# Performance work log

Hardware: AMD Instinct MI355X
Metric: run time of the kernel (lower is better)

The kernel has to match this reference:

```python
import jax, jax.numpy as jnp
import numpy as np
from jax import lax

B, T, C = 64, 50000, 4
MSYN, D, PATCH = 4, 160, 25
K_ENV, K_BUR, K_PRE = 25, 9, 9
DN = ('NCW', 'OIW', 'NCW')


def _dwconv(x, w, pad):
    # depthwise conv1d, x: [B,C,T], w: [C,1,K]
    return lax.conv_general_dilated(x, w, (1,), [(pad, pad)],
                                    dimension_numbers=DN,
                                    feature_group_count=x.shape[1])


def setup_inputs() -> dict:
    key = jax.random.key(0)
    ks = jax.random.split(key, 8)
    X = jax.random.normal(ks[0], (B, T, C), dtype=jnp.float32)
    M = jnp.ones((B, T, C), dtype=jnp.float32)
    s = 0.1
    w_env = jax.random.normal(ks[1], (C, 1, K_ENV), dtype=jnp.float32) * s
    w_burst = jax.random.normal(ks[2], (C, 1, K_BUR), dtype=jnp.float32) * s
    synergy_raw = jax.random.normal(ks[3], (MSYN, C), dtype=jnp.float32) * s
    w_pre_dw = jax.random.normal(ks[4], (MSYN, 1, K_PRE), dtype=jnp.float32) * s
    w_pre_pw = jax.random.normal(ks[5], (MSYN, MSYN, 1), dtype=jnp.float32) * s
    w_proj = jax.random.normal(ks[6], (D, MSYN, PATCH), dtype=jnp.float32) * s
    ln_gamma = jnp.ones((D,), dtype=jnp.float32)
    ln_beta = jnp.zeros((D,), dtype=jnp.float32)
    return {"X": X, "M": M, "w_env": w_env, "w_burst": w_burst,
            "synergy_raw": synergy_raw, "w_pre_dw": w_pre_dw,
            "w_pre_pw": w_pre_pw, "w_proj": w_proj,
            "ln_gamma": ln_gamma, "ln_beta": ln_beta}


def reference(X, M, w_env, w_burst, synergy_raw, w_pre_dw, w_pre_pw, w_proj, ln_gamma, ln_beta):
    # x: [B,C,T]
    x = (X * M).transpose(0, 2, 1)
    env = _dwconv(jnp.abs(x), w_env, K_ENV // 2)
    dx = jnp.pad(x[:, :, 1:] - x[:, :, :-1], ((0, 0), (0, 0), (1, 0)))
    burst = _dwconv(jnp.abs(dx), w_burst, K_BUR // 2)
    xm = 0.9 * env + 0.6 * burst + 0.2 * x
    # row-normalized softplus synergy matrix [Msyn, C]
    W = jax.nn.softplus(synergy_raw)
    W = W / jnp.maximum(W.sum(axis=1, keepdims=True), 1e-6)
    S = jnp.einsum('mc,bct->bmt', W, xm)
    Mm = (M.transpose(0, 2, 1) > 0).astype(x.dtype)
    Sm = jnp.clip(jnp.einsum('mc,bct->bmt', W, Mm), 0.0, 1.0)
    # pre: depthwise conv k=9 -> GELU -> 1x1 conv -> GELU (dropout = identity in eval)
    S = jax.nn.gelu(_dwconv(S, w_pre_dw, K_PRE // 2), approximate=False)
    S = jax.nn.gelu(jnp.einsum('om,bmt->bot', w_pre_pw[:, :, 0], S), approximate=False)
    S = S.transpose(0, 2, 1)          # [B,T,Msyn]
    Sm = Sm.transpose(0, 2, 1)        # [B,T,Msyn]
    # PatchProject1D
    p = PATCH
    T2 = (S.shape[1] // p) * p
    S = S[:, :T2, :]
    Sm = Sm[:, :T2, :]
    xs = (S * Sm).transpose(0, 2, 1)  # [B,Msyn,T2]
    h = lax.conv_general_dilated(xs, w_proj, (p,), 'VALID',
                                 dimension_numbers=DN).transpose(0, 2, 1)  # [B,L,D]
    mu = h.mean(axis=-1, keepdims=True)
    var = ((h - mu) ** 2).mean(axis=-1, keepdims=True)
    h = (h - mu) * lax.rsqrt(var + 1e-5) * ln_gamma + ln_beta
    # patchify time mask
    m_time = (Sm.mean(axis=-1) > 0).astype(jnp.float32)       # [B,T2]
    L = T2 // p
    m_patch = (m_time.reshape(Sm.shape[0], L, p).mean(axis=-1) > 0.1).astype(jnp.float32)
    return (h, m_patch)
```

## Files before the change

kernel.cpp:

```cpp
#include <hip/hip_runtime.h>
#include <hip/hip_bf16.h>
#include <cstddef>

#define T_LEN 50000

typedef __attribute__((ext_vector_type(8))) short bf16x8;
typedef __attribute__((ext_vector_type(4))) float f32x4;

__device__ __forceinline__ float sp_(float x){ return (x > 20.f) ? x : log1pf(expf(x)); }
__device__ __forceinline__ float gelu1(float x){ return 0.5f*x*(1.f + erff(x*0.7071067811865475f)); }

__global__ void k_cvtw(const float* __restrict__ wproj, __hip_bfloat16* __restrict__ wbf)
{
    int idx = blockIdx.x*256 + threadIdx.x;
    if (idx < 160*128) {
        int d = idx >> 7, i = idx & 127;
        float v = (i < 100) ? wproj[d*100 + i] : 0.f;
        wbf[idx] = __float2bfloat16(v);
    }
}

__global__ __launch_bounds__(256) void k_pre(
    const float* __restrict__ X, const float* __restrict__ Mq,
    const float* __restrict__ w_env, const float* __restrict__ w_bur,
    const float* __restrict__ syn, const float* __restrict__ wdw,
    const float* __restrict__ wpw,
    __hip_bfloat16* __restrict__ xs_out, float* __restrict__ mpatch)
{
    __shared__ float4 xb[1290];
    __shared__ float4 s1b[1134];
    __shared__ unsigned char maskb[1032];
    __shared__ float WnL[16];
    __shared__ float4 SmLUT[16];
    __shared__ __align__(16) __hip_bfloat16 abf[40*128];

    const int tid  = threadIdx.x;
    const int b    = blockIdx.x / 50;
    const int tile = blockIdx.x % 50;
    const int t0   = tile * 1000;

    const float4* X4 = (const float4*)X + (size_t)b * T_LEN;
    const float4* M4 = (const float4*)Mq + (size_t)b * T_LEN;
    #pragma unroll
    for (int jj = 0; jj < 5; ++jj) {
        int idx = tid + jj*256;
        if (idx < 1032) {
            int t = t0 - 16 + idx;
            float4 xv = make_float4(0.f,0.f,0.f,0.f);
            unsigned mk = 0u;
            if (t >= 0 && t < T_LEN) {
                float4 a = X4[t], m = M4[t];
                xv = make_float4(a.x*m.x, a.y*m.y, a.z*m.z, a.w*m.w);
                mk = (m.x>0.f?1u:0u) | (m.y>0.f?2u:0u) | (m.z>0.f?4u:0u) | (m.w>0.f?8u:0u);
            }
            xb[idx + (idx>>2)] = xv;
            maskb[idx] = (unsigned char)mk;
        }
    }
    for (int idx = tid; idx < 40*28; idx += 256) {
        int p = idx / 28, i = 100 + idx % 28;
        abf[p*128 + i] = __float2bfloat16(0.f);
    }
    if (tid < 4) {
        float w0 = sp_(syn[tid*4+0]), w1 = sp_(syn[tid*4+1]);
        float w2 = sp_(syn[tid*4+2]), w3 = sp_(syn[tid*4+3]);
        float inv = 1.f / fmaxf(w0+w1+w2+w3, 1e-6f);
        WnL[tid*4+0]=w0*inv; WnL[tid*4+1]=w1*inv; WnL[tid*4+2]=w2*inv; WnL[tid*4+3]=w3*inv;
    }
    __syncthreads();
    if (tid < 16) {
        float sm[4];
        #pragma unroll
        for (int m=0;m<4;++m) {
            float a = 0.f;
            #pragma unroll
            for (int c=0;c<4;++c) if (tid & (1<<c)) a += WnL[m*4+c];
            sm[m] = fminf(a, 1.f);
        }
        SmLUT[tid] = make_float4(sm[0],sm[1],sm[2],sm[3]);
    }

    if (tid < 252) {
        float4 env[4], bur[4], xk[4];
        #pragma unroll
        for (int j=0;j<4;++j){ env[j]=make_float4(0,0,0,0); bur[j]=make_float4(0,0,0,0); }
        float4 xprev = make_float4(0,0,0,0);
        const int base  = 4*tid;
        const int gbase = t0 - 4 + 4*tid;
        #pragma unroll
        for (int s = -12; s <= 15; ++s) {
            int lt = base + (s+12);
            float4 xc = xb[lt + (lt>>2)];
            float4 ax = make_float4(fabsf(xc.x),fabsf(xc.y),fabsf(xc.z),fabsf(xc.w));
            if (s >= -4 && s <= 7) {
                int g = gbase + s;
                float4 dx;
                if (g <= 0 || g >= T_LEN) dx = make_float4(0,0,0,0);
                else dx = make_float4(xc.x-xprev.x, xc.y-xprev.y, xc.z-xprev.z, xc.w-xprev.w);
                float4 adx = make_float4(fabsf(dx.x),fabsf(dx.y),fabsf(dx.z),fabsf(dx.w));
                #pragma unroll
                for (int j=0;j<4;++j) {
                    int bk = s + 4 - j;
                    if (bk >= 0 && bk < 9) {
                        float b0=w_bur[bk], b1=w_bur[9+bk], b2=w_bur[18+bk], b3=w_bur[27+bk];
                        bur[j].x = fmaf(b0, adx.x, bur[j].x);
                        bur[j].y = fmaf(b1, adx.y, bur[j].y);
                        bur[j].z = fmaf(b2, adx.z, bur[j].z);
                        bur[j].w = fmaf(b3, adx.w, bur[j].w);
                    }
                }
            }
            #pragma unroll
            for (int j=0;j<4;++j) {
                int k = s + 12 - j;
                if (k >= 0 && k < 25) {
                    float e0=w_env[k], e1=w_env[25+k], e2=w_env[50+k], e3=w_env[75+k];
                    env[j].x = fmaf(e0, ax.x, env[j].x);
                    env[j].y = fmaf(e1, ax.y, env[j].y);
                    env[j].z = fmaf(e2, ax.z, env[j].z);
                    env[j].w = fmaf(e3, ax.w, env[j].w);
                }
            }
            if (s >= 0 && s <= 3) xk[s] = xc;
            xprev = xc;
        }
        #pragma unroll
        for (int j=0;j<4;++j) {
            int g = gbase + j;
            float4 xm = make_float4(
                0.9f*env[j].x + 0.6f*bur[j].x + 0.2f*xk[j].x,
                0.9f*env[j].y + 0.6f*bur[j].y + 0.2f*xk[j].y,
                0.9f*env[j].z + 0.6f*bur[j].z + 0.2f*xk[j].z,
                0.9f*env[j].w + 0.6f*bur[j].w + 0.2f*xk[j].w);
            float4 out = make_float4(0,0,0,0);
            if (g >= 0 && g < T_LEN) {
                out.x = WnL[0]*xm.x  + WnL[1]*xm.y  + WnL[2]*xm.z  + WnL[3]*xm.w;
                out.y = WnL[4]*xm.x  + WnL[5]*xm.y  + WnL[6]*xm.z  + WnL[7]*xm.w;
                out.z = WnL[8]*xm.x  + WnL[9]*xm.y  + WnL[10]*xm.z + WnL[11]*xm.w;
                out.w = WnL[12]*xm.x + WnL[13]*xm.y + WnL[14]*xm.z + WnL[15]*xm.w;
            }
            int ls = base + j;
            s1b[ls + (ls>>3)] = out;
        }
    }
    __syncthreads();

    if (tid < 250) {
        float4 s2a[4];
        #pragma unroll
        for (int j=0;j<4;++j) s2a[j]=make_float4(0,0,0,0);
        const int base = 4*tid;
        #pragma unroll
        for (int s = -4; s <= 7; ++s) {
            int ls = base + s + 4;
            float4 sc = s1b[ls + (ls>>3)];
            #pragma unroll
            for (int j=0;j<4;++j) {
                int k = s + 4 - j;
                if (k >= 0 && k < 9) {
                    float d0=wdw[k], d1=wdw[9+k], d2=wdw[18+k], d3=wdw[27+k];
                    s2a[j].x = fmaf(d0, sc.x, s2a[j].x);
                    s2a[j].y = fmaf(d1, sc.y, s2a[j].y);
                    s2a[j].z = fmaf(d2, sc.z, s2a[j].z);
                    s2a[j].w = fmaf(d3, sc.w, s2a[j].w);
                }
            }
        }
        #pragma unroll
        for (int j=0;j<4;++j) {
            int t = base + j;
            float g0 = gelu1(s2a[j].x), g1 = gelu1(s2a[j].y);
            float g2 = gelu1(s2a[j].z), g3 = gelu1(s2a[j].w);
            float4 sm = SmLUT[maskb[t + 16]];
            int p = t / 25, k = t % 25;
            float smv[4] = {sm.x, sm.y, sm.z, sm.w};
            #pragma unroll
            for (int o=0;o<4;++o) {
                float v = wpw[o*4+0]*g0 + wpw[o*4+1]*g1 + wpw[o*4+2]*g2 + wpw[o*4+3]*g3;
                abf[p*128 + o*25 + k] = __float2bfloat16(gelu1(v) * smv[o]);
            }
        }
    }
    __syncthreads();

    {
        const float4* src = (const float4*)abf;
        float4* dst = (float4*)(xs_out + (size_t)(b*2000 + tile*40)*128);
        #pragma unroll
        for (int it = 0; it < 3; ++it) {
            int idx = tid + it*256;
            if (idx < 640) dst[idx] = src[idx];
        }
    }
    if (tid < 40) {
        int cnt = 0;
        #pragma unroll
        for (int k=0;k<25;++k) cnt += (maskb[16 + tid*25 + k] != 0) ? 1 : 0;
        mpatch[(size_t)b*2000 + tile*40 + tid] = (cnt >= 3) ? 1.f : 0.f;
    }
}

__global__ __launch_bounds__(256) void k_proj(
    const __hip_bfloat16* __restrict__ wbf, const __hip_bfloat16* __restrict__ xsg,
    const float* __restrict__ gamma, const float* __restrict__ beta,
    float* __restrict__ hout)
{
    __shared__ __align__(16) unsigned short Wl[160*136];
    __shared__ __align__(16) unsigned short Al[64*136];
    const int tid  = threadIdx.x;
    const int wv   = tid >> 6, lane = tid & 63;
    const int n    = lane & 15, quad = lane >> 4;

    {
        const float4* wg = (const float4*)wbf;
        #pragma unroll
        for (int it = 0; it < 10; ++it) {
            int idx = tid + it*256;
            int row = idx >> 4, cir = idx & 15;
            *(float4*)(Wl + row*136 + cir*8) = wg[idx];
        }
    }

    for (int bt = 0; bt < 2; ++bt) {
        const int p0 = (blockIdx.x*2 + bt) * 64;
        __syncthreads();
        {
            const float4* ag = (const float4*)(xsg + (size_t)p0*128);
            #pragma unroll
            for (int it = 0; it < 4; ++it) {
                int idx = tid + it*256;
                int row = idx >> 4, cir = idx & 15;
                *(float4*)(Al + row*136 + cir*8) = ag[idx];
            }
        }
        __syncthreads();

        f32x4 acc[10];
        #pragma unroll
        for (int t = 0; t < 10; ++t) acc[t] = (f32x4){0.f,0.f,0.f,0.f};
        #pragma unroll
        for (int kk = 0; kk < 4; ++kk) {
            bf16x8 pf = *(const bf16x8*)(Al + (wv*16 + n)*136 + kk*32 + quad*8);
            #pragma unroll
            for (int t = 0; t < 10; ++t) {
                bf16x8 wf = *(const bf16x8*)(Wl + (t*16 + n)*136 + kk*32 + quad*8);
                acc[t] = __builtin_amdgcn_mfma_f32_16x16x32_bf16(wf, pf, acc[t], 0, 0, 0);
            }
        }

        float s = 0.f;
        #pragma unroll
        for (int t = 0; t < 10; ++t) {
            #pragma unroll
            for (int r = 0; r < 4; ++r) s += acc[t][r];
        }
        s += __shfl_xor(s, 16, 64); s += __shfl_xor(s, 32, 64);
        const float mu = s * (1.f/160.f);
        float q = 0.f;
        #pragma unroll
        for (int t = 0; t < 10; ++t) {
            #pragma unroll
            for (int r = 0; r < 4; ++r) { float dv = acc[t][r] - mu; q = fmaf(dv, dv, q); }
        }
        q += __shfl_xor(q, 16, 64); q += __shfl_xor(q, 32, 64);
        const float rs = rsqrtf(q * (1.f/160.f) + 1e-5f);

        const int prow = p0 + wv*16 + n;
        float* hp = hout + (size_t)prow*160;
        #pragma unroll
        for (int t = 0; t < 10; ++t) {
            const float4 g  = *(const float4*)(gamma + t*16 + quad*4);
            const float4 be = *(const float4*)(beta  + t*16 + quad*4);
            float4 o;
            o.x = (acc[t][0] - mu)*rs*g.x + be.x;
            o.y = (acc[t][1] - mu)*rs*g.y + be.y;
            o.z = (acc[t][2] - mu)*rs*g.z + be.z;
            o.w = (acc[t][3] - mu)*rs*g.w + be.w;
            *(float4*)(hp + t*16 + quad*4) = o;
        }
    }
}

extern "C" void kernel_launch(void* const* d_in, const int* in_sizes, int n_in,
                              void* d_out, int out_size, void* d_ws, size_t ws_size,
                              hipStream_t stream) {
    const float* X     = (const float*)d_in[0];
    const float* M     = (const float*)d_in[1];
    const float* w_env = (const float*)d_in[2];
    const float* w_bur = (const float*)d_in[3];
    const float* syn   = (const float*)d_in[4];
    const float* wdw   = (const float*)d_in[5];
    const float* wpw   = (const float*)d_in[6];
    const float* wproj = (const float*)d_in[7];
    const float* gam   = (const float*)d_in[8];
    const float* bet   = (const float*)d_in[9];

    float* h      = (float*)d_out;
    float* mpatch = h + (size_t)64*2000*160;

    __hip_bfloat16* wbf = (__hip_bfloat16*)d_ws;
    __hip_bfloat16* xsb = (__hip_bfloat16*)((char*)d_ws + 65536);

    k_cvtw<<<80, 256, 0, stream>>>(wproj, wbf);
    k_pre<<<3200, 256, 0, stream>>>(X, M, w_env, w_bur, syn, wdw, wpw, xsb, mpatch);
    k_proj<<<1000, 256, 0, stream>>>(wbf, xsb, gam, bet, h);
}
```

Before: 257.5 us.

## Fuse patch projection and LayerNorm into the preprocessing kernel

```diff
diff --git a/kernel.cpp b/kernel.cpp
--- a/kernel.cpp
+++ b/kernel.cpp
@@ -20,19 +20,22 @@
     }
 }
 
-__global__ __launch_bounds__(256) void k_pre(
+__global__ __launch_bounds__(256, 2) void k_fused(
     const float* __restrict__ X, const float* __restrict__ Mq,
     const float* __restrict__ w_env, const float* __restrict__ w_bur,
     const float* __restrict__ syn, const float* __restrict__ wdw,
-    const float* __restrict__ wpw,
-    __hip_bfloat16* __restrict__ xs_out, float* __restrict__ mpatch)
+    const float* __restrict__ wpw, const __hip_bfloat16* __restrict__ wbf,
+    const float* __restrict__ gamma, const float* __restrict__ beta,
+    float* __restrict__ hout, float* __restrict__ mpatch)
 {
     __shared__ float4 xb[1290];
     __shared__ float4 s1b[1134];
     __shared__ unsigned char maskb[1032];
     __shared__ float WnL[16];
     __shared__ float4 SmLUT[16];
-    __shared__ __align__(16) __hip_bfloat16 abf[40*128];
+    __shared__ __align__(16) __hip_bfloat16 abf[48*136];
+    __shared__ float partS[4][3][16];
+    __shared__ float partQ[4][3][16];
 
     const int tid  = threadIdx.x;
     const int b    = blockIdx.x / 50;
@@ -57,9 +60,11 @@
             maskb[idx] = (unsigned char)mk;
         }
     }
-    for (int idx = tid; idx < 40*28; idx += 256) {
-        int p = idx / 28, i = 100 + idx % 28;
-        abf[p*128 + i] = __float2bfloat16(0.f);
+    for (int idx = tid; idx < 1120 + 1024; idx += 256) {
+        int p, i;
+        if (idx < 1120) { p = idx / 28; i = 100 + idx % 28; }
+        else { int j = idx - 1120; p = 40 + (j >> 7); i = j & 127; }
+        abf[p*136 + i] = __float2bfloat16(0.f);
     }
     if (tid < 4) {
         float w0 = sp_(syn[tid*4+0]), w1 = sp_(syn[tid*4+1]);
@@ -177,107 +182,116 @@
             #pragma unroll
             for (int o=0;o<4;++o) {
                 float v = wpw[o*4+0]*g0 + wpw[o*4+1]*g1 + wpw[o*4+2]*g2 + wpw[o*4+3]*g3;
-                abf[p*128 + o*25 + k] = __float2bfloat16(gelu1(v) * smv[o]);
+                abf[p*136 + o*25 + k] = __float2bfloat16(gelu1(v) * smv[o]);
             }
         }
     }
     __syncthreads();
 
     {
-        const float4* src = (const float4*)abf;
-        float4* dst = (float4*)(xs_out + (size_t)(b*2000 + tile*40)*128);
-        #pragma unroll
-        for (int it = 0; it < 3; ++it) {
-            int idx = tid + it*256;
-            if (idx < 640) dst[idx] = src[idx];
-        }
-    }
+        const int lane = tid & 63;
+        const int wv   = tid >> 6;
+        const int n    = lane & 15, quad = lane >> 4;
+        const int ndt  = (wv < 2) ? 3 : 2;
+        const int dt0  = (wv < 2) ? wv*3 : 6 + (wv-2)*2;
+
+        bf16x8 wf[3][4];
+        #pragma unroll
+        for (int i = 0; i < 3; ++i) {
+            if (i < ndt) {
+                const __hip_bfloat16* wr = wbf + (size_t)((dt0+i)*16 + n)*128 + quad*8;
+                #pragma unroll
+                for (int kk = 0; kk < 4; ++kk) wf[i][kk] = *(const bf16x8*)(wr + kk*32);
+            }
+        }
+
+        f32x4 acc[3][3];
+        #pragma unroll
+        for (int i=0;i<3;++i) {
+            #pragma unroll
+            for (int pt=0;pt<3;++pt) acc[i][pt] = (f32x4){0.f,0.f,0.f,0.f};
+        }
+        #pragma unroll
+        for (int kk = 0; kk < 4; ++kk) {
+            const bf16x8 pf0 = *(const bf16x8*)(abf + ( 0+n)*136 + kk*32 + quad*8);
+            const bf16x8 pf1 = *(const bf16x8*)(abf + (16+n)*136 + kk*32 + quad*8);
+            const bf16x8 pf2 = *(const bf16x8*)(abf + (32+n)*136 + kk*32 + quad*8);
+            #pragma unroll
+            for (int i = 0; i < 3; ++i) {
+                if (i < ndt) {
+                    acc[i][0] = __builtin_amdgcn_mfma_f32_16x16x32_bf16(wf[i][kk], pf0, acc[i][0], 0, 0, 0);
+                    acc[i][1] = __builtin_amdgcn_mfma_f32_16x16x32_bf16(wf[i][kk], pf1, acc[i][1], 0, 0, 0);
+                    acc[i][2] = __builtin_amdgcn_mfma_f32_16x16x32_bf16(wf[i][kk], pf2, acc[i][2], 0, 0, 0);
+                }
+            }
+        }
+
+        float mu[3];
+        #pragma unroll
+        for (int pt = 0; pt < 3; ++pt) {
+            float s = 0.f;
+            #pragma unroll
+            for (int i = 0; i < 3; ++i) {
+                if (i < ndt) {
+                    #pragma unroll
+                    for (int r = 0; r < 4; ++r) s += acc[i][pt][r];
+                }
+            }
+            s += __shfl_xor(s, 16, 64); s += __shfl_xor(s, 32, 64);
+            if (quad == 0) partS[wv][pt][n] = s;
+        }
+        __syncthreads();
+        #pragma unroll
+        for (int pt = 0; pt < 3; ++pt)
+            mu[pt] = (partS[0][pt][n] + partS[1][pt][n] + partS[2][pt][n] + partS[3][pt][n]) * (1.f/160.f);
+
+        float rs[3];
+        #pragma unroll
+        for (int pt = 0; pt < 3; ++pt) {
+            float q = 0.f;
+            #pragma unroll
+            for (int i = 0; i < 3; ++i) {
+                if (i < ndt) {
+                    #pragma unroll
+                    for (int r = 0; r < 4; ++r) { float dv = acc[i][pt][r] - mu[pt]; q = fmaf(dv, dv, q); }
+                }
+            }
+            q += __shfl_xor(q, 16, 64); q += __shfl_xor(q, 32, 64);
+            if (quad == 0) partQ[wv][pt][n] = q;
+        }
+        __syncthreads();
+        #pragma unroll
+        for (int pt = 0; pt < 3; ++pt) {
+            float q = partQ[0][pt][n] + partQ[1][pt][n] + partQ[2][pt][n] + partQ[3][pt][n];
+            rs[pt] = rsqrtf(q * (1.f/160.f) + 1e-5f);
+        }
+
+        #pragma unroll
+        for (int pt = 0; pt < 3; ++pt) {
+            if (pt == 2 && n >= 8) continue;
+            float* hp = hout + (size_t)(b*2000 + tile*40 + pt*16 + n)*160;
+            #pragma unroll
+            for (int i = 0; i < 3; ++i) {
+                if (i < ndt) {
+                    const int d0 = (dt0+i)*16 + quad*4;
+                    const float4 g  = *(const float4*)(gamma + d0);
+                    const float4 be = *(const float4*)(beta  + d0);
+                    float4 o;
+                    o.x = (acc[i][pt][0] - mu[pt])*rs[pt]*g.x + be.x;
+                    o.y = (acc[i][pt][1] - mu[pt])*rs[pt]*g.y + be.y;
+                    o.z = (acc[i][pt][2] - mu[pt])*rs[pt]*g.z + be.z;
+                    o.w = (acc[i][pt][3] - mu[pt])*rs[pt]*g.w + be.w;
+                    *(float4*)(hp + d0) = o;
+                }
+            }
+        }
+    }
+
     if (tid < 40) {
         int cnt = 0;
         #pragma unroll
         for (int k=0;k<25;++k) cnt += (maskb[16 + tid*25 + k] != 0) ? 1 : 0;
         mpatch[(size_t)b*2000 + tile*40 + tid] = (cnt >= 3) ? 1.f : 0.f;
-    }
-}
-
-__global__ __launch_bounds__(256) void k_proj(
-    const __hip_bfloat16* __restrict__ wbf, const __hip_bfloat16* __restrict__ xsg,
-    const float* __restrict__ gamma, const float* __restrict__ beta,
-    float* __restrict__ hout)
-{
-    __shared__ __align__(16) unsigned short Wl[160*136];
-    __shared__ __align__(16) unsigned short Al[64*136];
-    const int tid  = threadIdx.x;
-    const int wv   = tid >> 6, lane = tid & 63;
-    const int n    = lane & 15, quad = lane >> 4;
-
-    {
-        const float4* wg = (const float4*)wbf;
-        #pragma unroll
-        for (int it = 0; it < 10; ++it) {
-            int idx = tid + it*256;
-            int row = idx >> 4, cir = idx & 15;
-            *(float4*)(Wl + row*136 + cir*8) = wg[idx];
-        }
-    }
-
-    for (int bt = 0; bt < 2; ++bt) {
-        const int p0 = (blockIdx.x*2 + bt) * 64;
-        __syncthreads();
-        {
-            const float4* ag = (const float4*)(xsg + (size_t)p0*128);
-            #pragma unroll
-            for (int it = 0; it < 4; ++it) {
-                int idx = tid + it*256;
-                int row = idx >> 4, cir = idx & 15;
-                *(float4*)(Al + row*136 + cir*8) = ag[idx];
-            }
-        }
-        __syncthreads();
-
-        f32x4 acc[10];
-        #pragma unroll
-        for (int t = 0; t < 10; ++t) acc[t] = (f32x4){0.f,0.f,0.f,0.f};
-        #pragma unroll
-        for (int kk = 0; kk < 4; ++kk) {
-            bf16x8 pf = *(const bf16x8*)(Al + (wv*16 + n)*136 + kk*32 + quad*8);
-            #pragma unroll
-            for (int t = 0; t < 10; ++t) {
-                bf16x8 wf = *(const bf16x8*)(Wl + (t*16 + n)*136 + kk*32 + quad*8);
-                acc[t] = __builtin_amdgcn_mfma_f32_16x16x32_bf16(wf, pf, acc[t], 0, 0, 0);
-            }
-        }
-
-        float s = 0.f;
-        #pragma unroll
-        for (int t = 0; t < 10; ++t) {
-            #pragma unroll
-            for (int r = 0; r < 4; ++r) s += acc[t][r];
-        }
-        s += __shfl_xor(s, 16, 64); s += __shfl_xor(s, 32, 64);
-        const float mu = s * (1.f/160.f);
-        float q = 0.f;
-        #pragma unroll
-        for (int t = 0; t < 10; ++t) {
-            #pragma unroll
-            for (int r = 0; r < 4; ++r) { float dv = acc[t][r] - mu; q = fmaf(dv, dv, q); }
-        }
-        q += __shfl_xor(q, 16, 64); q += __shfl_xor(q, 32, 64);
-        const float rs = rsqrtf(q * (1.f/160.f) + 1e-5f);
-
-        const int prow = p0 + wv*16 + n;
-        float* hp = hout + (size_t)prow*160;
-        #pragma unroll
-        for (int t = 0; t < 10; ++t) {
-            const float4 g  = *(const float4*)(gamma + t*16 + quad*4);
-            const float4 be = *(const float4*)(beta  + t*16 + quad*4);
-            float4 o;
-            o.x = (acc[t][0] - mu)*rs*g.x + be.x;
-            o.y = (acc[t][1] - mu)*rs*g.y + be.y;
-            o.z = (acc[t][2] - mu)*rs*g.z + be.z;
-            o.w = (acc[t][3] - mu)*rs*g.w + be.w;
-            *(float4*)(hp + t*16 + quad*4) = o;
-        }
     }
 }
 
@@ -299,9 +313,7 @@
     float* mpatch = h + (size_t)64*2000*160;
 
     __hip_bfloat16* wbf = (__hip_bfloat16*)d_ws;
-    __hip_bfloat16* xsb = (__hip_bfloat16*)((char*)d_ws + 65536);
 
     k_cvtw<<<80, 256, 0, stream>>>(wproj, wbf);
-    k_pre<<<3200, 256, 0, stream>>>(X, M, w_env, w_bur, syn, wdw, wpw, xsb, mpatch);
-    k_proj<<<1000, 256, 0, stream>>>(wbf, xsb, gam, bet, h);
+    k_fused<<<3200, 256, 0, stream>>>(X, M, w_env, w_bur, syn, wdw, wpw, wbf, gam, bet, h, mpatch);
 }
```

Measured after the change: 267.2 us. 1.04x slower.

## Read X/M directly from global in k_pre, drop LDS staging and precompute synergy tables

Applied to the files above, without the earlier changes.

```diff
diff --git a/kernel.cpp b/kernel.cpp
--- a/kernel.cpp
+++ b/kernel.cpp
@@ -10,7 +10,9 @@
 __device__ __forceinline__ float sp_(float x){ return (x > 20.f) ? x : log1pf(expf(x)); }
 __device__ __forceinline__ float gelu1(float x){ return 0.5f*x*(1.f + erff(x*0.7071067811865475f)); }
 
-__global__ void k_cvtw(const float* __restrict__ wproj, __hip_bfloat16* __restrict__ wbf)
+__global__ void k_cvtw(const float* __restrict__ wproj, const float* __restrict__ syn,
+                       __hip_bfloat16* __restrict__ wbf, float* __restrict__ wn_g,
+                       float* __restrict__ sm_g)
 {
     int idx = blockIdx.x*256 + threadIdx.x;
     if (idx < 160*128) {
@@ -18,20 +20,115 @@
         float v = (i < 100) ? wproj[d*100 + i] : 0.f;
         wbf[idx] = __float2bfloat16(v);
     }
+    if (blockIdx.x == 0 && threadIdx.x < 16) {
+        float wn[16];
+        #pragma unroll
+        for (int m=0;m<4;++m){
+            float w0=sp_(syn[m*4+0]), w1=sp_(syn[m*4+1]);
+            float w2=sp_(syn[m*4+2]), w3=sp_(syn[m*4+3]);
+            float inv = 1.f/fmaxf(w0+w1+w2+w3, 1e-6f);
+            wn[m*4+0]=w0*inv; wn[m*4+1]=w1*inv; wn[m*4+2]=w2*inv; wn[m*4+3]=w3*inv;
+        }
+        wn_g[threadIdx.x] = wn[threadIdx.x];
+        const int mk = threadIdx.x;
+        #pragma unroll
+        for (int m=0;m<4;++m){
+            float a = 0.f;
+            #pragma unroll
+            for (int c=0;c<4;++c) if (mk & (1<<c)) a += wn[m*4+c];
+            sm_g[mk*4+m] = fminf(a, 1.f);
+        }
+    }
+}
+
+template<bool GUARD>
+__device__ __forceinline__ void phase2_body(
+    const float4* __restrict__ X4, const float4* __restrict__ M4,
+    int t0, int tid,
+    const float* __restrict__ w_env, const float* __restrict__ w_bur,
+    const float* __restrict__ wn,
+    float4* s1b, unsigned char* maskb)
+{
+    float4 env[4], bur[4], xk[4];
+    #pragma unroll
+    for (int j=0;j<4;++j){ env[j]=make_float4(0,0,0,0); bur[j]=make_float4(0,0,0,0); }
+    float4 xprev = make_float4(0,0,0,0);
+    const int base  = 4*tid;
+    const int gbase = t0 - 4 + 4*tid;
+    #pragma unroll
+    for (int s = -12; s <= 15; ++s) {
+        const int g = gbase + s;
+        float4 a = make_float4(0,0,0,0), m = make_float4(0,0,0,0);
+        if (!GUARD || (g >= 0 && g < T_LEN)) { a = X4[g]; m = M4[g]; }
+        const float4 xc = make_float4(a.x*m.x, a.y*m.y, a.z*m.z, a.w*m.w);
+        const float4 ax = make_float4(fabsf(xc.x),fabsf(xc.y),fabsf(xc.z),fabsf(xc.w));
+        if (s >= -4 && s <= 7) {
+            float4 dx;
+            if (GUARD && (g <= 0 || g >= T_LEN)) dx = make_float4(0,0,0,0);
+            else dx = make_float4(xc.x-xprev.x, xc.y-xprev.y, xc.z-xprev.z, xc.w-xprev.w);
+            const float4 adx = make_float4(fabsf(dx.x),fabsf(dx.y),fabsf(dx.z),fabsf(dx.w));
+            #pragma unroll
+            for (int j=0;j<4;++j) {
+                int bk = s + 4 - j;
+                if (bk >= 0 && bk < 9) {
+                    float b0=w_bur[bk], b1=w_bur[9+bk], b2=w_bur[18+bk], b3=w_bur[27+bk];
+                    bur[j].x = fmaf(b0, adx.x, bur[j].x);
+                    bur[j].y = fmaf(b1, adx.y, bur[j].y);
+                    bur[j].z = fmaf(b2, adx.z, bur[j].z);
+                    bur[j].w = fmaf(b3, adx.w, bur[j].w);
+                }
+            }
+        }
+        #pragma unroll
+        for (int j=0;j<4;++j) {
+            int k = s + 12 - j;
+            if (k >= 0 && k < 25) {
+                float e0=w_env[k], e1=w_env[25+k], e2=w_env[50+k], e3=w_env[75+k];
+                env[j].x = fmaf(e0, ax.x, env[j].x);
+                env[j].y = fmaf(e1, ax.y, env[j].y);
+                env[j].z = fmaf(e2, ax.z, env[j].z);
+                env[j].w = fmaf(e3, ax.w, env[j].w);
+            }
+        }
+        if (s >= 0 && s <= 3) {
+            xk[s] = xc;
+            const int lt = base - 4 + s;
+            if (lt >= 0 && lt < 1000) {
+                unsigned mk = (m.x>0.f?1u:0u) | (m.y>0.f?2u:0u) | (m.z>0.f?4u:0u) | (m.w>0.f?8u:0u);
+                maskb[lt] = (unsigned char)mk;
+            }
+        }
+        xprev = xc;
+    }
+    #pragma unroll
+    for (int j=0;j<4;++j) {
+        const int g = gbase + j;
+        float4 xm = make_float4(
+            0.9f*env[j].x + 0.6f*bur[j].x + 0.2f*xk[j].x,
+            0.9f*env[j].y + 0.6f*bur[j].y + 0.2f*xk[j].y,
+            0.9f*env[j].z + 0.6f*bur[j].z + 0.2f*xk[j].z,
+            0.9f*env[j].w + 0.6f*bur[j].w + 0.2f*xk[j].w);
+        float4 out = make_float4(0,0,0,0);
+        if (g >= 0 && g < T_LEN) {
+            out.x = wn[0]*xm.x  + wn[1]*xm.y  + wn[2]*xm.z  + wn[3]*xm.w;
+            out.y = wn[4]*xm.x  + wn[5]*xm.y  + wn[6]*xm.z  + wn[7]*xm.w;
+            out.z = wn[8]*xm.x  + wn[9]*xm.y  + wn[10]*xm.z + wn[11]*xm.w;
+            out.w = wn[12]*xm.x + wn[13]*xm.y + wn[14]*xm.z + wn[15]*xm.w;
+        }
+        const int ls = base + j;
+        s1b[ls + (ls>>3)] = out;
+    }
 }
 
 __global__ __launch_bounds__(256) void k_pre(
     const float* __restrict__ X, const float* __restrict__ Mq,
     const float* __restrict__ w_env, const float* __restrict__ w_bur,
-    const float* __restrict__ syn, const float* __restrict__ wdw,
-    const float* __restrict__ wpw,
+    const float* __restrict__ wdw, const float* __restrict__ wpw,
+    const float* __restrict__ wn_g, const float* __restrict__ sm_g,
     __hip_bfloat16* __restrict__ xs_out, float* __restrict__ mpatch)
 {
-    __shared__ float4 xb[1290];
     __shared__ float4 s1b[1134];
-    __shared__ unsigned char maskb[1032];
-    __shared__ float WnL[16];
-    __shared__ float4 SmLUT[16];
+    __shared__ unsigned char maskb[1000];
     __shared__ __align__(16) __hip_bfloat16 abf[40*128];
 
     const int tid  = threadIdx.x;
@@ -41,111 +138,21 @@
 
     const float4* X4 = (const float4*)X + (size_t)b * T_LEN;
     const float4* M4 = (const float4*)Mq + (size_t)b * T_LEN;
-    #pragma unroll
-    for (int jj = 0; jj < 5; ++jj) {
-        int idx = tid + jj*256;
-        if (idx < 1032) {
-            int t = t0 - 16 + idx;
-            float4 xv = make_float4(0.f,0.f,0.f,0.f);
-            unsigned mk = 0u;
-            if (t >= 0 && t < T_LEN) {
-                float4 a = X4[t], m = M4[t];
-                xv = make_float4(a.x*m.x, a.y*m.y, a.z*m.z, a.w*m.w);
-                mk = (m.x>0.f?1u:0u) | (m.y>0.f?2u:0u) | (m.z>0.f?4u:0u) | (m.w>0.f?8u:0u);
-            }
-            xb[idx + (idx>>2)] = xv;
-            maskb[idx] = (unsigned char)mk;
-        }
-    }
+
     for (int idx = tid; idx < 40*28; idx += 256) {
         int p = idx / 28, i = 100 + idx % 28;
         abf[p*128 + i] = __float2bfloat16(0.f);
     }
-    if (tid < 4) {
-        float w0 = sp_(syn[tid*4+0]), w1 = sp_(syn[tid*4+1]);
-        float w2 = sp_(syn[tid*4+2]), w3 = sp_(syn[tid*4+3]);
-        float inv = 1.f / fmaxf(w0+w1+w2+w3, 1e-6f);
-        WnL[tid*4+0]=w0*inv; WnL[tid*4+1]=w1*inv; WnL[tid*4+2]=w2*inv; WnL[tid*4+3]=w3*inv;
+
+    if (tid < 252) {
+        const bool interior = (tile != 0) && (tile != 49);
+        if (interior) phase2_body<false>(X4, M4, t0, tid, w_env, w_bur, wn_g, s1b, maskb);
+        else          phase2_body<true >(X4, M4, t0, tid, w_env, w_bur, wn_g, s1b, maskb);
     }
     __syncthreads();
-    if (tid < 16) {
-        float sm[4];
-        #pragma unroll
-        for (int m=0;m<4;++m) {
-            float a = 0.f;
-            #pragma unroll
-            for (int c=0;c<4;++c) if (tid & (1<<c)) a += WnL[m*4+c];
-            sm[m] = fminf(a, 1.f);
-        }
-        SmLUT[tid] = make_float4(sm[0],sm[1],sm[2],sm[3]);
-    }
-
-    if (tid < 252) {
-        float4 env[4], bur[4], xk[4];
-        #pragma unroll
-        for (int j=0;j<4;++j){ env[j]=make_float4(0,0,0,0); bur[j]=make_float4(0,0,0,0); }
-        float4 xprev = make_float4(0,0,0,0);
-        const int base  = 4*tid;
-        const int gbase = t0 - 4 + 4*tid;
-        #pragma unroll
-        for (int s = -12; s <= 15; ++s) {
-            int lt = base + (s+12);
-            float4 xc = xb[lt + (lt>>2)];
-            float4 ax = make_float4(fabsf(xc.x),fabsf(xc.y),fabsf(xc.z),fabsf(xc.w));
-            if (s >= -4 && s <= 7) {
-                int g = gbase + s;
-                float4 dx;
-                if (g <= 0 || g >= T_LEN) dx = make_float4(0,0,0,0);
-                else dx = make_float4(xc.x-xprev.x, xc.y-xprev.y, xc.z-xprev.z, xc.w-xprev.w);
-                float4 adx = make_float4(fabsf(dx.x),fabsf(dx.y),fabsf(dx.z),fabsf(dx.w));
-                #pragma unroll
-                for (int j=0;j<4;++j) {
-                    int bk = s + 4 - j;
-                    if (bk >= 0 && bk < 9) {
-                        float b0=w_bur[bk], b1=w_bur[9+bk], b2=w_bur[18+bk], b3=w_bur[27+bk];
-                        bur[j].x = fmaf(b0, adx.x, bur[j].x);
-                        bur[j].y = fmaf(b1, adx.y, bur[j].y);
-                        bur[j].z = fmaf(b2, adx.z, bur[j].z);
-                        bur[j].w = fmaf(b3, adx.w, bur[j].w);
-                    }
-                }
-            }
-            #pragma unroll
-            for (int j=0;j<4;++j) {
-                int k = s + 12 - j;
-                if (k >= 0 && k < 25) {
-                    float e0=w_env[k], e1=w_env[25+k], e2=w_env[50+k], e3=w_env[75+k];
-                    env[j].x = fmaf(e0, ax.x, env[j].x);
-                    env[j].y = fmaf(e1, ax.y, env[j].y);
-                    env[j].z = fmaf(e2, ax.z, env[j].z);
-                    env[j].w = fmaf(e3, ax.w, env[j].w);
-                }
-            }
-            if (s >= 0 && s <= 3) xk[s] = xc;
-            xprev = xc;
-        }
-        #pragma unroll
-        for (int j=0;j<4;++j) {
-            int g = gbase + j;
-            float4 xm = make_float4(
-                0.9f*env[j].x + 0.6f*bur[j].x + 0.2f*xk[j].x,
-                0.9f*env[j].y + 0.6f*bur[j].y + 0.2f*xk[j].y,
-                0.9f*env[j].z + 0.6f*bur[j].z + 0.2f*xk[j].z,
-                0.9f*env[j].w + 0.6f*bur[j].w + 0.2f*xk[j].w);
-            float4 out = make_float4(0,0,0,0);
-            if (g >= 0 && g < T_LEN) {
-                out.x = WnL[0]*xm.x  + WnL[1]*xm.y  + WnL[2]*xm.z  + WnL[3]*xm.w;
-                out.y = WnL[4]*xm.x  + WnL[5]*xm.y  + WnL[6]*xm.z  + WnL[7]*xm.w;
-                out.z = WnL[8]*xm.x  + WnL[9]*xm.y  + WnL[10]*xm.z + WnL[11]*xm.w;
-                out.w = WnL[12]*xm.x + WnL[13]*xm.y + WnL[14]*xm.z + WnL[15]*xm.w;
-            }
-            int ls = base + j;
-            s1b[ls + (ls>>3)] = out;
-        }
-    }
-    __syncthreads();
 
     if (tid < 250) {
+        const float4* sm4 = (const float4*)sm_g;
         float4 s2a[4];
         #pragma unroll
         for (int j=0;j<4;++j) s2a[j]=make_float4(0,0,0,0);
@@ -171,7 +178,7 @@
             int t = base + j;
             float g0 = gelu1(s2a[j].x), g1 = gelu1(s2a[j].y);
             float g2 = gelu1(s2a[j].z), g3 = gelu1(s2a[j].w);
-            float4 sm = SmLUT[maskb[t + 16]];
+            float4 sm = sm4[maskb[t]];
             int p = t / 25, k = t % 25;
             float smv[4] = {sm.x, sm.y, sm.z, sm.w};
             #pragma unroll
@@ -195,7 +202,7 @@
     if (tid < 40) {
         int cnt = 0;
         #pragma unroll
-        for (int k=0;k<25;++k) cnt += (maskb[16 + tid*25 + k] != 0) ? 1 : 0;
+        for (int k=0;k<25;++k) cnt += (maskb[tid*25 + k] != 0) ? 1 : 0;
         mpatch[(size_t)b*2000 + tile*40 + tid] = (cnt >= 3) ? 1.f : 0.f;
     }
 }
@@ -299,9 +306,11 @@
     float* mpatch = h + (size_t)64*2000*160;
 
     __hip_bfloat16* wbf = (__hip_bfloat16*)d_ws;
+    float* wn_g = (float*)((char*)d_ws + 40960);
+    float* sm_g = (float*)((char*)d_ws + 41024);
     __hip_bfloat16* xsb = (__hip_bfloat16*)((char*)d_ws + 65536);
 
-    k_cvtw<<<80, 256, 0, stream>>>(wproj, wbf);
-    k_pre<<<3200, 256, 0, stream>>>(X, M, w_env, w_bur, syn, wdw, wpw, xsb, mpatch);
+    k_cvtw<<<80, 256, 0, stream>>>(wproj, syn, wbf, wn_g, sm_g);
+    k_pre<<<3200, 256, 0, stream>>>(X, M, w_env, w_bur, wdw, wpw, wn_g, sm_g, xsb, mpatch);
     k_proj<<<1000, 256, 0, stream>>>(wbf, xsb, gam, bet, h);
 }
```

Result: slower. 309.3 us (+20.1%).

## Compute envelope and burst depthwise convs via banded-Toeplitz bf16 MFMA

Applied to the files above, without the earlier changes.

```diff
diff --git a/kernel.cpp b/kernel.cpp
--- a/kernel.cpp
+++ b/kernel.cpp
@@ -9,57 +9,99 @@
 
 __device__ __forceinline__ float sp_(float x){ return (x > 20.f) ? x : log1pf(expf(x)); }
 __device__ __forceinline__ float gelu1(float x){ return 0.5f*x*(1.f + erff(x*0.7071067811865475f)); }
-
-__global__ void k_cvtw(const float* __restrict__ wproj, __hip_bfloat16* __restrict__ wbf)
+__device__ __forceinline__ unsigned short f2bf(float x){
+    __hip_bfloat16 h = __float2bfloat16(x);
+    return *reinterpret_cast<unsigned short*>(&h);
+}
+
+__global__ void k_cvtw(const float* __restrict__ wproj, const float* __restrict__ w_env,
+                       const float* __restrict__ w_bur,
+                       __hip_bfloat16* __restrict__ wbf, __hip_bfloat16* __restrict__ ag)
 {
-    int idx = blockIdx.x*256 + threadIdx.x;
-    if (idx < 160*128) {
-        int d = idx >> 7, i = idx & 127;
+    int gid = blockIdx.x*256 + threadIdx.x;
+    if (gid < 160*128) {
+        int d = gid >> 7, i = gid & 127;
         float v = (i < 100) ? wproj[d*100 + i] : 0.f;
-        wbf[idx] = __float2bfloat16(v);
+        wbf[gid] = __float2bfloat16(v);
+    }
+    int idx2 = gid - 160*128;
+    if (idx2 >= 0 && idx2 < 12*512) {
+        int m = idx2 >> 9, rem = idx2 & 511, i = rem >> 5, j = rem & 31;
+        int ch = m & 3, ty = m >> 2;
+        float v = 0.f;
+        if (ty == 0)      { int k = j - i;      if (k >= 0 && k <= 24) v = w_env[ch*25 + k]; }
+        else if (ty == 1) { int k = j + 32 - i; if (k <= 24)           v = w_env[ch*25 + k]; }
+        else              { int k = j - i - 8;  if (k >= 0 && k <= 8)  v = w_bur[ch*9  + k]; }
+        ag[idx2] = __float2bfloat16(v);
     }
 }
 
 __global__ __launch_bounds__(256) void k_pre(
     const float* __restrict__ X, const float* __restrict__ Mq,
-    const float* __restrict__ w_env, const float* __restrict__ w_bur,
     const float* __restrict__ syn, const float* __restrict__ wdw,
-    const float* __restrict__ wpw,
+    const float* __restrict__ wpw, const __hip_bfloat16* __restrict__ ag,
     __hip_bfloat16* __restrict__ xs_out, float* __restrict__ mpatch)
 {
-    __shared__ float4 xb[1290];
+    __shared__ float4 xb[1152];
     __shared__ float4 s1b[1134];
-    __shared__ unsigned char maskb[1032];
+    __shared__ unsigned int mask4[272];
     __shared__ float WnL[16];
     __shared__ float4 SmLUT[16];
-    __shared__ __align__(16) __hip_bfloat16 abf[40*128];
+    __shared__ __align__(16) unsigned char upool[17408];
+    unsigned short* axb  = (unsigned short*)upool;
+    unsigned short* adxb = axb + 4*1088;
+    __hip_bfloat16* abf  = (__hip_bfloat16*)upool;
 
     const int tid  = threadIdx.x;
     const int b    = blockIdx.x / 50;
     const int tile = blockIdx.x % 50;
     const int t0   = tile * 1000;
+    unsigned char* maskb = (unsigned char*)mask4;
 
     const float4* X4 = (const float4*)X + (size_t)b * T_LEN;
     const float4* M4 = (const float4*)Mq + (size_t)b * T_LEN;
-    #pragma unroll
-    for (int jj = 0; jj < 5; ++jj) {
-        int idx = tid + jj*256;
-        if (idx < 1032) {
-            int t = t0 - 16 + idx;
-            float4 xv = make_float4(0.f,0.f,0.f,0.f);
-            unsigned mk = 0u;
+
+    for (int g0 = tid*4; g0 < 1088; g0 += 1024) {
+        float4 xv[5];
+        unsigned mk = 0u;
+        #pragma unroll
+        for (int e = 0; e < 5; ++e) {
+            int t = t0 - 17 + g0 + e;
+            float4 x = make_float4(0.f,0.f,0.f,0.f);
             if (t >= 0 && t < T_LEN) {
                 float4 a = X4[t], m = M4[t];
-                xv = make_float4(a.x*m.x, a.y*m.y, a.z*m.z, a.w*m.w);
-                mk = (m.x>0.f?1u:0u) | (m.y>0.f?2u:0u) | (m.z>0.f?4u:0u) | (m.w>0.f?8u:0u);
-            }
-            xb[idx + (idx>>2)] = xv;
-            maskb[idx] = (unsigned char)mk;
-        }
-    }
-    for (int idx = tid; idx < 40*28; idx += 256) {
-        int p = idx / 28, i = 100 + idx % 28;
-        abf[p*128 + i] = __float2bfloat16(0.f);
+                x = make_float4(a.x*m.x, a.y*m.y, a.z*m.z, a.w*m.w);
+                if (e >= 1) {
+                    unsigned mb = (m.x>0.f?1u:0u)|(m.y>0.f?2u:0u)|(m.z>0.f?4u:0u)|(m.w>0.f?8u:0u);
+                    mk |= mb << ((e-1)*8);
+                }
+            }
+            xv[e] = x;
+        }
+        mask4[g0>>2] = mk;
+        #pragma unroll
+        for (int e = 1; e < 5; ++e) {
+            int u = g0 + e - 13;
+            if (u >= 0 && u < 1024) xb[u + (u>>3)] = xv[e];
+        }
+        unsigned short ua[4][4], ud[4][4];
+        #pragma unroll
+        for (int e = 1; e < 5; ++e) {
+            int gt = t0 - 16 + g0 + (e-1);
+            float4 x = xv[e], xp = xv[e-1];
+            bool dv = (gt >= 1 && gt < T_LEN);
+            float d0 = dv ? x.x - xp.x : 0.f, d1 = dv ? x.y - xp.y : 0.f;
+            float d2 = dv ? x.z - xp.z : 0.f, d3 = dv ? x.w - xp.w : 0.f;
+            ua[0][e-1] = f2bf(fabsf(x.x)); ua[1][e-1] = f2bf(fabsf(x.y));
+            ua[2][e-1] = f2bf(fabsf(x.z)); ua[3][e-1] = f2bf(fabsf(x.w));
+            ud[0][e-1] = f2bf(fabsf(d0));  ud[1][e-1] = f2bf(fabsf(d1));
+            ud[2][e-1] = f2bf(fabsf(d2));  ud[3][e-1] = f2bf(fabsf(d3));
+        }
+        #pragma unroll
+        for (int c = 0; c < 4; ++c) {
+            *(ushort4*)(axb  + c*1088 + g0) = make_ushort4(ua[c][0],ua[c][1],ua[c][2],ua[c][3]);
+            *(ushort4*)(adxb + c*1088 + g0) = make_ushort4(ud[c][0],ud[c][1],ud[c][2],ud[c][3]);
+        }
     }
     if (tid < 4) {
         float w0 = sp_(syn[tid*4+0]), w1 = sp_(syn[tid*4+1]);
@@ -80,75 +122,59 @@
         SmLUT[tid] = make_float4(sm[0],sm[1],sm[2],sm[3]);
     }
 
-    if (tid < 252) {
-        float4 env[4], bur[4], xk[4];
-        #pragma unroll
-        for (int j=0;j<4;++j){ env[j]=make_float4(0,0,0,0); bur[j]=make_float4(0,0,0,0); }
-        float4 xprev = make_float4(0,0,0,0);
-        const int base  = 4*tid;
-        const int gbase = t0 - 4 + 4*tid;
-        #pragma unroll
-        for (int s = -12; s <= 15; ++s) {
-            int lt = base + (s+12);
-            float4 xc = xb[lt + (lt>>2)];
-            float4 ax = make_float4(fabsf(xc.x),fabsf(xc.y),fabsf(xc.z),fabsf(xc.w));
-            if (s >= -4 && s <= 7) {
-                int g = gbase + s;
-                float4 dx;
-                if (g <= 0 || g >= T_LEN) dx = make_float4(0,0,0,0);
-                else dx = make_float4(xc.x-xprev.x, xc.y-xprev.y, xc.z-xprev.z, xc.w-xprev.w);
-                float4 adx = make_float4(fabsf(dx.x),fabsf(dx.y),fabsf(dx.z),fabsf(dx.w));
-                #pragma unroll
-                for (int j=0;j<4;++j) {
-                    int bk = s + 4 - j;
-                    if (bk >= 0 && bk < 9) {
-                        float b0=w_bur[bk], b1=w_bur[9+bk], b2=w_bur[18+bk], b3=w_bur[27+bk];
-                        bur[j].x = fmaf(b0, adx.x, bur[j].x);
-                        bur[j].y = fmaf(b1, adx.y, bur[j].y);
-                        bur[j].z = fmaf(b2, adx.z, bur[j].z);
-                        bur[j].w = fmaf(b3, adx.w, bur[j].w);
-                    }
+    {
+        const int lane = tid & 63, wv = tid >> 6;
+        const int n = lane & 15, q = lane >> 4;
+        bf16x8 A1[4], A2[4], Ab[4];
+        #pragma unroll
+        for (int c = 0; c < 4; ++c) {
+            A1[c] = *(const bf16x8*)(ag + (c   )*512 + n*32 + q*8);
+            A2[c] = *(const bf16x8*)(ag + (4+c )*512 + n*32 + q*8);
+            Ab[c] = *(const bf16x8*)(ag + (8+c )*512 + n*32 + q*8);
+        }
+        const int jb = 256*wv + 16*n;
+        f32x4 ea[4], ba[4];
+        #pragma unroll
+        for (int c = 0; c < 4; ++c) {
+            bf16x8 B1 = *(const bf16x8*)(axb  + c*1088 + jb      + q*8);
+            bf16x8 B2 = *(const bf16x8*)(axb  + c*1088 + jb + 32 + q*8);
+            bf16x8 Bb = *(const bf16x8*)(adxb + c*1088 + jb      + q*8);
+            f32x4 z = (f32x4){0.f,0.f,0.f,0.f};
+            z     = __builtin_amdgcn_mfma_f32_16x16x32_bf16(A1[c], B1, z, 0, 0, 0);
+            ea[c] = __builtin_amdgcn_mfma_f32_16x16x32_bf16(A2[c], B2, z, 0, 0, 0);
+            ba[c] = __builtin_amdgcn_mfma_f32_16x16x32_bf16(Ab[c], Bb, (f32x4){0.f,0.f,0.f,0.f}, 0, 0, 0);
+        }
+        #pragma unroll
+        for (int r = 0; r < 4; ++r) {
+            const int u = 256*wv + 16*n + 4*q + r;
+            if (u < 1008) {
+                const int g = t0 - 4 + u;
+                float4 out = make_float4(0.f,0.f,0.f,0.f);
+                if (g >= 0 && g < T_LEN) {
+                    float4 x = xb[u + (u>>3)];
+                    float m0 = 0.9f*ea[0][r] + 0.6f*ba[0][r] + 0.2f*x.x;
+                    float m1 = 0.9f*ea[1][r] + 0.6f*ba[1][r] + 0.2f*x.y;
+                    float m2 = 0.9f*ea[2][r] + 0.6f*ba[2][r] + 0.2f*x.z;
+                    float m3 = 0.9f*ea[3][r] + 0.6f*ba[3][r] + 0.2f*x.w;
+                    out.x = WnL[0]*m0  + WnL[1]*m1  + WnL[2]*m2  + WnL[3]*m3;
+                    out.y = WnL[4]*m0  + WnL[5]*m1  + WnL[6]*m2  + WnL[7]*m3;
+                    out.z = WnL[8]*m0  + WnL[9]*m1  + WnL[10]*m2 + WnL[11]*m3;
+                    out.w = WnL[12]*m0 + WnL[13]*m1 + WnL[14]*m2 + WnL[15]*m3;
                 }
-            }
-            #pragma unroll
-            for (int j=0;j<4;++j) {
-                int k = s + 12 - j;
-                if (k >= 0 && k < 25) {
-                    float e0=w_env[k], e1=w_env[25+k], e2=w_env[50+k], e3=w_env[75+k];
-                    env[j].x = fmaf(e0, ax.x, env[j].x);
-                    env[j].y = fmaf(e1, ax.y, env[j].y);
-                    env[j].z = fmaf(e2, ax.z, env[j].z);
-                    env[j].w = fmaf(e3, ax.w, env[j].w);
-                }
-            }
-            if (s >= 0 && s <= 3) xk[s] = xc;
-            xprev = xc;
-        }
-        #pragma unroll
-        for (int j=0;j<4;++j) {
-            int g = gbase + j;
-            float4 xm = make_float4(
-                0.9f*env[j].x + 0.6f*bur[j].x + 0.2f*xk[j].x,
-                0.9f*env[j].y + 0.6f*bur[j].y + 0.2f*xk[j].y,
-                0.9f*env[j].z + 0.6f*bur[j].z + 0.2f*xk[j].z,
-                0.9f*env[j].w + 0.6f*bur[j].w + 0.2f*xk[j].w);
-            float4 out = make_float4(0,0,0,0);
-            if (g >= 0 && g < T_LEN) {
-                out.x = WnL[0]*xm.x  + WnL[1]*xm.y  + WnL[2]*xm.z  + WnL[3]*xm.w;
-                out.y = WnL[4]*xm.x  + WnL[5]*xm.y  + WnL[6]*xm.z  + WnL[7]*xm.w;
-                out.z = WnL[8]*xm.x  + WnL[9]*xm.y  + WnL[10]*xm.z + WnL[11]*xm.w;
-                out.w = WnL[12]*xm.x + WnL[13]*xm.y + WnL[14]*xm.z + WnL[15]*xm.w;
-            }
-            int ls = base + j;
-            s1b[ls + (ls>>3)] = out;
+                s1b[u + (u>>3)] = out;
+            }
         }
     }
     __syncthreads();
 
+    for (int idx = tid; idx < 40*28; idx += 256) {
+        int p = idx / 28, i = 100 + idx % 28;
+        abf[p*128 + i] = __float2bfloat16(0.f);
+    }
     if (tid < 250) {
         float4 s2a[4];
         #pragma unroll
-        for (int j=0;j<4;++j) s2a[j]=make_float4(0,0,0,0);
+        for (int j=0;j<4;++j) s2a[j]=make_float4(0.f,0.f,0.f,0.f);
         const int base = 4*tid;
         #pragma unroll
         for (int s = -4; s <= 7; ++s) {
@@ -225,12 +251,12 @@
         const int p0 = (blockIdx.x*2 + bt) * 64;
         __syncthreads();
         {
-            const float4* ag = (const float4*)(xsg + (size_t)p0*128);
+            const float4* ag2 = (const float4*)(xsg + (size_t)p0*128);
             #pragma unroll
             for (int it = 0; it < 4; ++it) {
                 int idx = tid + it*256;
                 int row = idx >> 4, cir = idx & 15;
-                *(float4*)(Al + row*136 + cir*8) = ag[idx];
+                *(float4*)(Al + row*136 + cir*8) = ag2[idx];
             }
         }
         __syncthreads();
@@ -299,9 +325,10 @@
     float* mpatch = h + (size_t)64*2000*160;
 
     __hip_bfloat16* wbf = (__hip_bfloat16*)d_ws;
+    __hip_bfloat16* agm = (__hip_bfloat16*)((char*)d_ws + 40960);
     __hip_bfloat16* xsb = (__hip_bfloat16*)((char*)d_ws + 65536);
 
-    k_cvtw<<<80, 256, 0, stream>>>(wproj, wbf);
-    k_pre<<<3200, 256, 0, stream>>>(X, M, w_env, w_bur, syn, wdw, wpw, xsb, mpatch);
+    k_cvtw<<<104, 256, 0, stream>>>(wproj, w_env, w_bur, wbf, agm);
+    k_pre<<<3200, 256, 0, stream>>>(X, M, syn, wdw, wpw, agm, xsb, mpatch);
     k_proj<<<1000, 256, 0, stream>>>(wbf, xsb, gam, bet, h);
 }
```

Result: faster. 248.1 us (-3.6%).
